# Kernel optimization log

Measured on AMD Instinct MI355X. Metric: run time of the kernel, lower is better.

Reference implementation:

```python
import jax, jax.numpy as jnp
import numpy as np
import math

B, NOUT, NCLASSES, CENTER, TOPK = 1024, 512, 5994, 3, 5
M, SUB_M, SCALE = 0.2, -0.06, 30.0

COS_M, SIN_M = math.cos(M), math.sin(M)
TH, MM = math.cos(math.pi - M), math.sin(math.pi - M) * M
SUB_COS_M, SUB_SIN_M = math.cos(SUB_M), math.sin(SUB_M)
SUB_TH, SUB_MM = math.cos(math.pi - SUB_M), math.sin(math.pi - SUB_M) * SUB_M


def setup_inputs() -> dict:
    key = jax.random.key(0)
    k1, k2, k3 = jax.random.split(key, 3)
    x = jax.random.normal(k1, (B, NOUT), dtype=jnp.float32)
    # xavier_normal over (center, nClasses, nOut): fan_in=nClasses*nOut, fan_out=center*nOut
    std = math.sqrt(2.0 / (NCLASSES * NOUT + CENTER * NOUT))
    weight = jax.random.normal(k2, (CENTER, NCLASSES, NOUT), dtype=jnp.float32) * std
    label = jax.random.randint(k3, (B,), 0, NCLASSES, dtype=jnp.int64)
    return {"x": x, "weight": weight, "label": label}


def _l2norm(v, axis=-1, eps=1e-12):
    return v / jnp.maximum(jnp.linalg.norm(v, axis=axis, keepdims=True), eps)


def reference(x, weight, label):
    xn = _l2norm(x)                       # [B, j]
    wn = _l2norm(weight)                  # [a, c, j]
    cosine_subcen = jnp.einsum('bj,acj->bac', xn, wn)   # [B, center, C]
    cosine = jnp.max(cosine_subcen, axis=1)             # [B, C]

    sine = jnp.sqrt(jnp.clip(1.0 - cosine * cosine, 0.0, 1.0))
    phi = jnp.where(cosine - TH > 0, cosine * COS_M - sine * SIN_M, cosine - MM)
    sub_phi = jnp.where(cosine - SUB_TH > 0,
                        cosine * SUB_COS_M - sine * SUB_SIN_M,
                        cosine - SUB_MM)

    # topk+1 candidates; drop the label column if present, else drop the last
    _, idx = jax.lax.top_k(cosine, TOPK + 1)            # [B, topk+1]
    is_label = (idx == label[:, None].astype(idx.dtype))
    # stable sort pushes the (unique) label hit to the end, preserving order otherwise
    order = jnp.argsort(is_label.astype(jnp.int32), axis=1, stable=True)
    idx_fixed = jnp.take_along_axis(idx, order[:, :TOPK], axis=1)   # [B, topk]

    rows = jnp.arange(B)[:, None]
    one_hot_sub = jnp.zeros_like(cosine).at[rows, idx_fixed].add(1.0)
    one_hot = jax.nn.one_hot(label, NCLASSES, dtype=cosine.dtype)

    output = (one_hot * phi + one_hot_sub * sub_phi
              + (1.0 - one_hot_sub - one_hot) * cosine) * SCALE

    logp = jax.nn.log_softmax(output, axis=-1)
    loss = -jnp.mean(logp[jnp.arange(B), label])

    pred = jnp.argmax(cosine * SCALE, axis=-1)
    prec1 = jnp.mean((pred == label).astype(jnp.float32)) * 100.0
    return loss, prec1
```

## Files before the change

### kernel.cpp

```cpp
#include <hip/hip_runtime.h>
#include <math.h>

#define NB 1024
#define NC 5994
#define NCP 6144
#define NK 512
#define NA 3
#define NT2 24
#define SCALE_F 30.0f
#define NPT 24

#define COS_M_F 0.9800665778412416f
#define SIN_M_F 0.19866933079506122f
#define TH_F (-0.9800665778412416f)
#define MM_F 0.039733866159012244f
#define SUB_COS_M_F 0.9982005399352042f
#define SUB_SIN_M_F (-0.05996400647944459f)
#define SUB_TH_F (-0.9982005399352042f)
#define SUB_MM_F 0.0035978403887666754f

typedef __attribute__((ext_vector_type(8))) short short8;
typedef __attribute__((ext_vector_type(4))) float f32x4;

__device__ __forceinline__ float waveReduceSum(float v) {
#pragma unroll
  for (int off = 32; off > 0; off >>= 1) v += __shfl_down(v, off);
  return v;
}

__device__ __forceinline__ void waveArgMax(float& v, int& i) {
#pragma unroll
  for (int off = 32; off > 0; off >>= 1) {
    float ov = __shfl_down(v, off);
    int oi = __shfl_down(i, off);
    if (ov > v || (ov == v && (unsigned)oi < (unsigned)i)) { v = ov; i = oi; }
  }
}

__device__ __forceinline__ ushort f2bf(float f) {
  unsigned u = __float_as_uint(f);
  u += 0x7FFFu + ((u >> 16) & 1u);
  return (ushort)(u >> 16);
}

__device__ __forceinline__ void load_lds16(const ushort* g, ushort* l) {
  __builtin_amdgcn_global_load_lds(
      (const __attribute__((address_space(1))) unsigned int*)g,
      (__attribute__((address_space(3))) unsigned int*)l, 16, 0, 0);
}

__global__ __launch_bounds__(256) void norm_convert(const float* __restrict__ x,
                                                    const float* __restrict__ w,
                                                    ushort* __restrict__ xb,
                                                    ushort* __restrict__ wb) {
  const int row = blockIdx.x * 4 + (threadIdx.x >> 6);
  const int lane = threadIdx.x & 63;
  const float* src;
  ushort* dst;
  if (row < NB) {
    src = x + (size_t)row * NK;
    dst = xb + (size_t)row * NK;
  } else {
    const int r = row - NB;
    const int a = r / NCP, c = r % NCP;
    dst = wb + (size_t)r * NK;
    if (c >= NC) {
      ushort4 z = {0, 0, 0, 0};
      *(ushort4*)(dst + lane * 4) = z;
      *(ushort4*)(dst + 256 + lane * 4) = z;
      return;
    }
    src = w + ((size_t)a * NC + c) * NK;
  }
  const float4 v0 = *(const float4*)(src + lane * 4);
  const float4 v1 = *(const float4*)(src + 256 + lane * 4);
  float ss = v0.x * v0.x + v0.y * v0.y + v0.z * v0.z + v0.w * v0.w +
             v1.x * v1.x + v1.y * v1.y + v1.z * v1.z + v1.w * v1.w;
  ss = waveReduceSum(ss);
  ss = __shfl(ss, 0);
  const float rn = 1.0f / fmaxf(sqrtf(ss), 1e-12f);
  ushort4 o0 = {f2bf(v0.x * rn), f2bf(v0.y * rn), f2bf(v0.z * rn), f2bf(v0.w * rn)};
  ushort4 o1 = {f2bf(v1.x * rn), f2bf(v1.y * rn), f2bf(v1.z * rn), f2bf(v1.w * rn)};
  *(ushort4*)(dst + lane * 4) = o0;
  *(ushort4*)(dst + 256 + lane * 4) = o1;
}

__global__ __launch_bounds__(128) void cos_gemm_mfma(const ushort* __restrict__ Xb,
                                                     const ushort* __restrict__ Wb,
                                                     float* __restrict__ cosine) {
  __shared__ ushort sA0[64 * 64];
  __shared__ ushort sA1[64 * 64];
  __shared__ ushort sB0[128 * 64];
  __shared__ ushort sB1[128 * 64];
  const int tid = threadIdx.x;
  const int lane = tid & 63;
  const int w = tid >> 6;

  const int id = blockIdx.x;
  const int cx = (id & 7) + ((id >> 7) << 3);
  const int by = (id >> 3) & 15;
  const int b0 = by * 64;
  const int c0 = cx * 128;

  const int lrow = lane >> 2;
  const int skg = ((lane & 3) - ((lane >> 3) & 3)) & 3;
  const ushort* gA = Xb + (size_t)(b0 + w * 32 + lrow) * NK + skg * 8;
  const ushort* gB = Wb + (size_t)(c0 + w * 64 + lrow) * NK + skg * 8;
  const int w4 = w * 4;

  const int r = lane & 15;
  const int kg = lane >> 4;
  const int rdoff = r * 32 + (((kg + (r >> 1)) & 3) * 8);

  f32x4 best[4][4];
  f32x4 acc[4][4];
#pragma unroll
  for (int i = 0; i < 4; ++i)
#pragma unroll
    for (int j = 0; j < 4; ++j) {
#pragma unroll
      for (int q = 0; q < 4; ++q) best[i][j][q] = -INFINITY;
      acc[i][j] = (f32x4)(0.f);
    }

#define STAGE(TT, SAw, SBw)                                                     \
  {                                                                             \
    const int tt_ = (TT);                                                       \
    const int kb = (tt_ & 7) << 6;                                              \
    const size_t boff = (size_t)(tt_ >> 3) * NCP * NK + kb;                     \
    _Pragma("unroll") for (int kk = 0; kk < 2; ++kk) {                          \
      _Pragma("unroll") for (int s = 0; s < 2; ++s)                             \
          load_lds16(gA + (size_t)s * 16 * NK + kb + kk * 32,                   \
                     (ushort*)SAw + (kk * 4 + 2 * w + s) * 512);                \
      _Pragma("unroll") for (int j = 0; j < 4; ++j)                             \
          load_lds16(gB + boff + (size_t)j * 16 * NK + kk * 32,                 \
                     (ushort*)SBw + (kk * 8 + w4 + j) * 512);                   \
    }                                                                           \
  }

  STAGE(0, sA0, sB0)
  __syncthreads();

#define GEMM_BODY(T, SAr, SBr, SAw, SBw)                                        \
  {                                                                             \
    const int t_ = (T);                                                         \
    if (t_ + 1 < NT2) STAGE(t_ + 1, SAw, SBw)                                   \
    short8 af[4][2], bf[4][2];                                                  \
    _Pragma("unroll") for (int kk = 0; kk < 2; ++kk) {                          \
      _Pragma("unroll") for (int mi = 0; mi < 4; ++mi)                          \
          af[mi][kk] = *(const short8*)&SAr[(kk * 4 + mi) * 512 + rdoff];       \
      _Pragma("unroll") for (int ni = 0; ni < 4; ++ni)                          \
          bf[ni][kk] = *(const short8*)&SBr[(kk * 8 + w4 + ni) * 512 + rdoff];  \
    }                                                                           \
    _Pragma("unroll") for (int kk = 0; kk < 2; ++kk)                            \
        _Pragma("unroll") for (int mi = 0; mi < 4; ++mi)                        \
            _Pragma("unroll") for (int ni = 0; ni < 4; ++ni)                    \
                acc[mi][ni] = __builtin_amdgcn_mfma_f32_16x16x32_bf16(          \
                    af[mi][kk], bf[ni][kk], acc[mi][ni], 0, 0, 0);              \
    if ((t_ & 7) == 7) {                                                        \
      _Pragma("unroll") for (int i = 0; i < 4; ++i)                             \
          _Pragma("unroll") for (int j = 0; j < 4; ++j) {                       \
        _Pragma("unroll") for (int q = 0; q < 4; ++q)                           \
            best[i][j][q] = fmaxf(best[i][j][q], acc[i][j][q]);                 \
        acc[i][j] = (f32x4)(0.f);                                               \
      }                                                                         \
    }                                                                           \
    __syncthreads();                                                            \
  }

  for (int t = 0; t < NT2; t += 2) {
    GEMM_BODY(t, sA0, sB0, sA1, sB1)
    GEMM_BODY(t + 1, sA1, sB1, sA0, sB0)
  }
#undef GEMM_BODY
#undef STAGE

  const int q4 = (lane >> 4) * 4;
#pragma unroll
  for (int ni = 0; ni < 4; ++ni) {
    const int col = c0 + w * 64 + ni * 16 + r;
    if (col < NC) {
#pragma unroll
      for (int mi = 0; mi < 4; ++mi) {
        const int row0 = b0 + mi * 16 + q4;
#pragma unroll
        for (int q = 0; q < 4; ++q)
          cosine[(size_t)(row0 + q) * NC + col] = best[mi][ni][q];
      }
    }
  }
}

__global__ __launch_bounds__(256) void row_loss(const float* __restrict__ cosine,
                                                const int* __restrict__ label,
                                                float* __restrict__ loss_b,
                                                float* __restrict__ corr_b) {
  __shared__ float swv[4];
  __shared__ int swi[4];
  __shared__ float s_red[4];
  __shared__ float s_maxv;
  __shared__ float s_cosL;
  __shared__ float topv[6];
  __shared__ int topi[6];

  const int b = blockIdx.x, tid = threadIdx.x;
  const int wv = tid >> 6;
  const int lab = label[b];
  const float* row = cosine + (size_t)b * NC;

  float v[NPT];
  float bv = -INFINITY;
  int bi = -1;
#pragma unroll
  for (int j = 0; j < NPT; ++j) {
    const int i = tid + j * 256;
    v[j] = (i < NC) ? row[i] : -INFINITY;
    if (v[j] > bv) { bv = v[j]; bi = i; }
  }
  if (tid == (lab & 255)) s_cosL = v[lab >> 8];
  waveArgMax(bv, bi);
  if ((tid & 63) == 0) { swv[wv] = bv; swi[wv] = bi; }
  __syncthreads();
  if (tid == 0) {
    float mv = swv[0]; int mi = swi[0];
    for (int q = 1; q < 4; ++q)
      if (swv[q] > mv || (swv[q] == mv && (unsigned)swi[q] < (unsigned)mi)) { mv = swv[q]; mi = swi[q]; }
    s_maxv = mv; topv[0] = mv; topi[0] = mi;
  }
  __syncthreads();
  const float maxv = s_maxv;

  float ps = 0.f;
#pragma unroll
  for (int j = 0; j < NPT; ++j) ps += __expf(SCALE_F * (v[j] - maxv));
  ps = waveReduceSum(ps);
  if ((tid & 63) == 0) s_red[wv] = ps;

  unsigned excl = 0;
  {
    const int wi = topi[0];
    if ((wi & 255) == tid) excl |= 1u << (wi >> 8);
  }

  for (int e = 1; e < 6; ++e) {
    float lv = -INFINITY;
    int li = -1;
#pragma unroll
    for (int j = 0; j < NPT; ++j)
      if (!((excl >> j) & 1u) && v[j] > lv) { lv = v[j]; li = tid + j * 256; }
    waveArgMax(lv, li);
    if ((tid & 63) == 0) { swv[wv] = lv; swi[wv] = li; }
    __syncthreads();
    if (tid == 0) {
      float mv = swv[0]; int mi = swi[0];
      for (int q = 1; q < 4; ++q)
        if (swv[q] > mv || (swv[q] == mv && (unsigned)swi[q] < (unsigned)mi)) { mv = swv[q]; mi = swi[q]; }
      topv[e] = mv; topi[e] = mi;
    }
    __syncthreads();
    const int wi = topi[e];
    if ((wi & 255) == tid) excl |= 1u << (wi >> 8);
  }

  if (tid == 0) {
    const float S = s_red[0] + s_red[1] + s_red[2] + s_red[3];
    const float m = SCALE_F * maxv;
    const float cosL = s_cosL;
    const float sineL = sqrtf(fminf(fmaxf(1.f - cosL * cosL, 0.f), 1.f));
    const float phiL = (cosL - TH_F > 0.f) ? (cosL * COS_M_F - sineL * SIN_M_F) : (cosL - MM_F);
    float adj = __expf(SCALE_F * phiL - m) - __expf(SCALE_F * cosL - m);
    int cnt = 0;
    for (int e = 0; e < 6 && cnt < 5; ++e) {
      if (topi[e] == lab) continue;
      const float c = topv[e];
      const float sine = sqrtf(fminf(fmaxf(1.f - c * c, 0.f), 1.f));
      const float sp = (c - SUB_TH_F > 0.f) ? (c * SUB_COS_M_F - sine * SUB_SIN_M_F) : (c - SUB_MM_F);
      adj += __expf(SCALE_F * sp - m) - __expf(SCALE_F * c - m);
      ++cnt;
    }
    const float Sp = S + adj;
    loss_b[b] = (logf(Sp) + m) - SCALE_F * phiL;
    corr_b[b] = (topi[0] == lab) ? 1.f : 0.f;
  }
}

__global__ __launch_bounds__(256) void finalize(const float* __restrict__ loss_b,
                                                const float* __restrict__ corr_b,
                                                float* __restrict__ out) {
  const int tid = threadIdx.x;
  float ls = 0.f, cs = 0.f;
  for (int i = tid; i < NB; i += 256) { ls += loss_b[i]; cs += corr_b[i]; }
  ls = waveReduceSum(ls);
  cs = waveReduceSum(cs);
  __shared__ float sl[4], sc[4];
  if ((tid & 63) == 0) { sl[tid >> 6] = ls; sc[tid >> 6] = cs; }
  __syncthreads();
  if (tid == 0) {
    const float L = sl[0] + sl[1] + sl[2] + sl[3];
    const float Cr = sc[0] + sc[1] + sc[2] + sc[3];
    out[0] = L / (float)NB;
    out[1] = Cr / (float)NB * 100.f;
  }
}

extern "C" void kernel_launch(void* const* d_in, const int* in_sizes, int n_in,
                              void* d_out, int out_size, void* d_ws, size_t ws_size,
                              hipStream_t stream) {
  const float* x = (const float*)d_in[0];
  const float* w = (const float*)d_in[1];
  const int* label = (const int*)d_in[2];
  float* out = (float*)d_out;
  char* ws = (char*)d_ws;

  ushort* xb = (ushort*)ws;
  ushort* wb = (ushort*)(ws + 1048576);
  float* cosine = (float*)(ws + 1048576 + 18874368);
  float* loss_b = (float*)ws;
  float* corr_b = (float*)(ws + 4096);

  norm_convert<<<(NB + NA * NCP) / 4, 256, 0, stream>>>(x, w, xb, wb);
  cos_gemm_mfma<<<16 * 48, 128, 0, stream>>>(xb, wb, cosine);
  row_loss<<<NB, 256, 0, stream>>>(cosine, label, loss_b, corr_b);
  finalize<<<1, 256, 0, stream>>>(loss_b, corr_b, out);
}
```

Measured before the change: 77.05 us.

## Halve GEMM column tile and store cosine matrix as bf16

The GEMM block tile shrinks from 64x128 to 64x64, with waves now split along rows instead of columns, and the grid doubles to 1536 blocks. This gives more blocks for better CU occupancy and load balance. The intermediate cosine matrix is written as bf16 rather than fp32, which halves the write and read traffic between the GEMM and the row-loss kernel. The cost is extra rounding of cosine values, which may change argmax ties and top-k selection and shifts the loss slightly. Smaller tiles also mean less operand reuse per block.

```diff
diff --git a/kernel.cpp b/kernel.cpp
--- a/kernel.cpp
+++ b/kernel.cpp
@@ -41,6 +41,10 @@
   unsigned u = __float_as_uint(f);
   u += 0x7FFFu + ((u >> 16) & 1u);
   return (ushort)(u >> 16);
+}
+
+__device__ __forceinline__ float bf2f(ushort u) {
+  return __uint_as_float(((unsigned)u) << 16);
 }
 
 __device__ __forceinline__ void load_lds16(const ushort* g, ushort* l) {
@@ -87,11 +91,11 @@
 
 __global__ __launch_bounds__(128) void cos_gemm_mfma(const ushort* __restrict__ Xb,
                                                      const ushort* __restrict__ Wb,
-                                                     float* __restrict__ cosine) {
+                                                     ushort* __restrict__ cosb) {
   __shared__ ushort sA0[64 * 64];
   __shared__ ushort sA1[64 * 64];
-  __shared__ ushort sB0[128 * 64];
-  __shared__ ushort sB1[128 * 64];
+  __shared__ ushort sB0[64 * 64];
+  __shared__ ushort sB1[64 * 64];
   const int tid = threadIdx.x;
   const int lane = tid & 63;
   const int w = tid >> 6;
@@ -100,22 +104,22 @@
   const int cx = (id & 7) + ((id >> 7) << 3);
   const int by = (id >> 3) & 15;
   const int b0 = by * 64;
-  const int c0 = cx * 128;
+  const int c0 = cx * 64;
 
   const int lrow = lane >> 2;
   const int skg = ((lane & 3) - ((lane >> 3) & 3)) & 3;
   const ushort* gA = Xb + (size_t)(b0 + w * 32 + lrow) * NK + skg * 8;
-  const ushort* gB = Wb + (size_t)(c0 + w * 64 + lrow) * NK + skg * 8;
-  const int w4 = w * 4;
+  const ushort* gB = Wb + (size_t)(c0 + w * 32 + lrow) * NK + skg * 8;
+  const int w2 = w * 2;
 
   const int r = lane & 15;
   const int kg = lane >> 4;
   const int rdoff = r * 32 + (((kg + (r >> 1)) & 3) * 8);
 
-  f32x4 best[4][4];
-  f32x4 acc[4][4];
-#pragma unroll
-  for (int i = 0; i < 4; ++i)
+  f32x4 best[2][4];
+  f32x4 acc[2][4];
+#pragma unroll
+  for (int i = 0; i < 2; ++i)
 #pragma unroll
     for (int j = 0; j < 4; ++j) {
 #pragma unroll
@@ -128,13 +132,12 @@
     const int tt_ = (TT);                                                       \
     const int kb = (tt_ & 7) << 6;                                              \
     const size_t boff = (size_t)(tt_ >> 3) * NCP * NK + kb;                     \
-    _Pragma("unroll") for (int kk = 0; kk < 2; ++kk) {                          \
-      _Pragma("unroll") for (int s = 0; s < 2; ++s)                             \
-          load_lds16(gA + (size_t)s * 16 * NK + kb + kk * 32,                   \
-                     (ushort*)SAw + (kk * 4 + 2 * w + s) * 512);                \
-      _Pragma("unroll") for (int j = 0; j < 4; ++j)                             \
-          load_lds16(gB + boff + (size_t)j * 16 * NK + kk * 32,                 \
-                     (ushort*)SBw + (kk * 8 + w4 + j) * 512);                   \
+    _Pragma("unroll") for (int kk = 0; kk < 2; ++kk)                            \
+        _Pragma("unroll") for (int g = 0; g < 2; ++g) {                         \
+      load_lds16(gA + (size_t)g * 16 * NK + kb + kk * 32,                       \
+                 (ushort*)SAw + (kk * 4 + w2 + g) * 512);                       \
+      load_lds16(gB + (size_t)g * 16 * NK + boff + kk * 32,                     \
+                 (ushort*)SBw + (kk * 4 + w2 + g) * 512);                       \
     }                                                                           \
   }
 
@@ -145,20 +148,20 @@
   {                                                                             \
     const int t_ = (T);                                                         \
     if (t_ + 1 < NT2) STAGE(t_ + 1, SAw, SBw)                                   \
-    short8 af[4][2], bf[4][2];                                                  \
+    short8 af[2][2], bf[4][2];                                                  \
     _Pragma("unroll") for (int kk = 0; kk < 2; ++kk) {                          \
-      _Pragma("unroll") for (int mi = 0; mi < 4; ++mi)                          \
-          af[mi][kk] = *(const short8*)&SAr[(kk * 4 + mi) * 512 + rdoff];       \
+      _Pragma("unroll") for (int mi = 0; mi < 2; ++mi)                          \
+          af[mi][kk] = *(const short8*)&SAr[(kk * 4 + w2 + mi) * 512 + rdoff];  \
       _Pragma("unroll") for (int ni = 0; ni < 4; ++ni)                          \
-          bf[ni][kk] = *(const short8*)&SBr[(kk * 8 + w4 + ni) * 512 + rdoff];  \
+          bf[ni][kk] = *(const short8*)&SBr[(kk * 4 + ni) * 512 + rdoff];       \
     }                                                                           \
     _Pragma("unroll") for (int kk = 0; kk < 2; ++kk)                            \
-        _Pragma("unroll") for (int mi = 0; mi < 4; ++mi)                        \
+        _Pragma("unroll") for (int mi = 0; mi < 2; ++mi)                        \
             _Pragma("unroll") for (int ni = 0; ni < 4; ++ni)                    \
                 acc[mi][ni] = __builtin_amdgcn_mfma_f32_16x16x32_bf16(          \
                     af[mi][kk], bf[ni][kk], acc[mi][ni], 0, 0, 0);              \
     if ((t_ & 7) == 7) {                                                        \
-      _Pragma("unroll") for (int i = 0; i < 4; ++i)                             \
+      _Pragma("unroll") for (int i = 0; i < 2; ++i)                             \
           _Pragma("unroll") for (int j = 0; j < 4; ++j) {                       \
         _Pragma("unroll") for (int q = 0; q < 4; ++q)                           \
             best[i][j][q] = fmaxf(best[i][j][q], acc[i][j][q]);                 \
@@ -178,20 +181,20 @@
   const int q4 = (lane >> 4) * 4;
 #pragma unroll
   for (int ni = 0; ni < 4; ++ni) {
-    const int col = c0 + w * 64 + ni * 16 + r;
+    const int col = c0 + ni * 16 + r;
     if (col < NC) {
 #pragma unroll
-      for (int mi = 0; mi < 4; ++mi) {
-        const int row0 = b0 + mi * 16 + q4;
+      for (int mi = 0; mi < 2; ++mi) {
+        const int row0 = b0 + w * 32 + mi * 16 + q4;
 #pragma unroll
         for (int q = 0; q < 4; ++q)
-          cosine[(size_t)(row0 + q) * NC + col] = best[mi][ni][q];
+          cosb[(size_t)(row0 + q) * NC + col] = f2bf(best[mi][ni][q]);
       }
     }
   }
 }
 
-__global__ __launch_bounds__(256) void row_loss(const float* __restrict__ cosine,
+__global__ __launch_bounds__(256) void row_loss(const ushort* __restrict__ cosb,
                                                 const int* __restrict__ label,
                                                 float* __restrict__ loss_b,
                                                 float* __restrict__ corr_b) {
@@ -206,7 +209,7 @@
   const int b = blockIdx.x, tid = threadIdx.x;
   const int wv = tid >> 6;
   const int lab = label[b];
-  const float* row = cosine + (size_t)b * NC;
+  const ushort* row = cosb + (size_t)b * NC;
 
   float v[NPT];
   float bv = -INFINITY;
@@ -214,7 +217,7 @@
 #pragma unroll
   for (int j = 0; j < NPT; ++j) {
     const int i = tid + j * 256;
-    v[j] = (i < NC) ? row[i] : -INFINITY;
+    v[j] = (i < NC) ? bf2f(row[i]) : -INFINITY;
     if (v[j] > bv) { bv = v[j]; bi = i; }
   }
   if (tid == (lab & 255)) s_cosL = v[lab >> 8];
@@ -314,12 +317,12 @@
 
   ushort* xb = (ushort*)ws;
   ushort* wb = (ushort*)(ws + 1048576);
-  float* cosine = (float*)(ws + 1048576 + 18874368);
+  ushort* cosb = (ushort*)(ws + 1048576 + 18874368);
   float* loss_b = (float*)ws;
   float* corr_b = (float*)(ws + 4096);
 
   norm_convert<<<(NB + NA * NCP) / 4, 256, 0, stream>>>(x, w, xb, wb);
-  cos_gemm_mfma<<<16 * 48, 128, 0, stream>>>(xb, wb, cosine);
-  row_loss<<<NB, 256, 0, stream>>>(cosine, label, loss_b, corr_b);
+  cos_gemm_mfma<<<16 * 96, 128, 0, stream>>>(xb, wb, cosb);
+  row_loss<<<NB, 256, 0, stream>>>(cosb, label, loss_b, corr_b);
   finalize<<<1, 256, 0, stream>>>(loss_b, corr_b, out);
 }
```

Result: faster. 70.45 us (-8.6%).
